# Kernel optimization log

Measured on AMD Instinct MI355X. Metric: run time of the kernel, lower is better.

Reference implementation:

```python
import jax, jax.numpy as jnp
import numpy as np

D_MODEL = 1024
N_HEAD = 16
HEAD_DIM = D_MODEL // N_HEAD


def setup_inputs() -> dict:
    key = jax.random.key(0)
    ks = jax.random.split(key, 11)
    B, S = 2, 2048
    scale = 1.0 / np.sqrt(D_MODEL)
    inp = {
        'q': jax.random.normal(ks[0], (B, S, D_MODEL), dtype=jnp.float32),
        'k': jax.random.normal(ks[1], (B, S, D_MODEL), dtype=jnp.float32),
        'v': jax.random.normal(ks[2], (B, S, D_MODEL), dtype=jnp.float32),
        'Wq': jax.random.normal(ks[3], (D_MODEL, D_MODEL), dtype=jnp.float32) * scale,
        'bq': jnp.zeros((D_MODEL,), dtype=jnp.float32),
        'Wk': jax.random.normal(ks[4], (D_MODEL, D_MODEL), dtype=jnp.float32) * scale,
        'bk': jnp.zeros((D_MODEL,), dtype=jnp.float32),
        'Wv': jax.random.normal(ks[5], (D_MODEL, D_MODEL), dtype=jnp.float32) * scale,
        'bv': jnp.zeros((D_MODEL,), dtype=jnp.float32),
        'Wo': jax.random.normal(ks[6], (D_MODEL, D_MODEL), dtype=jnp.float32) * scale,
        'bo': jnp.zeros((D_MODEL,), dtype=jnp.float32),
    }
    return inp


def _split_heads(x):
    # [B, S, D] -> [B, H, S, Dh]
    B, S, _ = x.shape
    return x.reshape(B, S, N_HEAD, HEAD_DIM).transpose(0, 2, 1, 3)


def reference(q, k, v, Wq, bq, Wk, bk, Wv, bv, Wo, bo):
    B, S, _ = q.shape
    qh = _split_heads(q @ Wq + bq)  # [B,H,S,Dh]
    kh = _split_heads(k @ Wk + bk)
    vh = _split_heads(v @ Wv + bv)
    inv_sqrt_d = jnp.asarray(1.0 / np.sqrt(HEAD_DIM), dtype=q.dtype)
    scores = jnp.einsum('bhqd,bhkd->bhqk', qh, kh) * inv_sqrt_d  # [B,H,S,S]
    attn = jax.nn.softmax(scores, axis=-1)
    out = jnp.einsum('bhqk,bhkd->bhqd', attn, vh)  # [B,H,S,Dh]
    out = out.transpose(0, 2, 1, 3).reshape(B, S, D_MODEL)
    return out @ Wo + bo
```

## Files before the change

### kernel.cpp

```cpp
#include <hip/hip_runtime.h>
#include <cstdint>
#include <cstddef>

#define D_MODEL 1024
#define NHEAD 16
#define HDIM 64
#define BATCH 2
#define SEQ 2048
#define MROWS (BATCH*SEQ)

typedef _Float16 f16;
typedef _Float16 f16x2 __attribute__((ext_vector_type(2)));
typedef _Float16 f16x4 __attribute__((ext_vector_type(4)));
typedef _Float16 f16x8 __attribute__((ext_vector_type(8)));
typedef float f32x4 __attribute__((ext_vector_type(4)));
typedef __fp16 fp16x2_raw __attribute__((ext_vector_type(2)));

__device__ __forceinline__ f16x2 cvt_pk(float a, float b) {
  fp16x2_raw t = __builtin_amdgcn_cvt_pkrtz(a, b);
  return __builtin_bit_cast(f16x2, t);
}

#define QSCALE 0.18033688011112042f
#define CSHIFT 6.0f

__device__ __forceinline__ void gload_lds16(const void* gsrc, void* ldst) {
  __builtin_amdgcn_global_load_lds(
      (__attribute__((address_space(1))) void*)gsrc,
      (__attribute__((address_space(3))) void*)ldst,
      16, 0, 0);
}

__global__ __launch_bounds__(256) void cast3_kernel(
    const float* __restrict__ q, const float* __restrict__ k,
    const float* __restrict__ v, f16* __restrict__ Xf) {
  const int z = blockIdx.y;
  const float* in = (z == 0) ? q : (z == 1) ? k : v;
  f16* out = Xf + (size_t)z * MROWS * D_MODEL;
  int i = (blockIdx.x * 256 + threadIdx.x) * 8;
  const float4* p = (const float4*)(in + i);
  float4 a = p[0], b = p[1];
  f16x8 o = { (f16)a.x,(f16)a.y,(f16)a.z,(f16)a.w,
              (f16)b.x,(f16)b.y,(f16)b.z,(f16)b.w };
  *(f16x8*)(out + i) = o;
}

__global__ __launch_bounds__(256) void transpose4_kernel(
    const float* __restrict__ W0, const float* __restrict__ W1,
    const float* __restrict__ W2, const float* __restrict__ W3,
    f16* __restrict__ T0, f16* __restrict__ T1,
    f16* __restrict__ T2, f16* __restrict__ T3) {
  const int z = blockIdx.z;
  const float* W = (z == 0) ? W0 : (z == 1) ? W1 : (z == 2) ? W2 : W3;
  f16* Wt = (z == 0) ? T0 : (z == 1) ? T1 : (z == 2) ? T2 : T3;
  __shared__ float tile[32][33];
  int n0 = blockIdx.x * 32, k0 = blockIdx.y * 32;
  int tx = threadIdx.x, ty = threadIdx.y;
  #pragma unroll
  for (int j = 0; j < 32; j += 8)
    tile[ty + j][tx] = W[(size_t)(k0 + ty + j) * D_MODEL + n0 + tx];
  __syncthreads();
  #pragma unroll
  for (int j = 0; j < 32; j += 8)
    Wt[(size_t)(n0 + ty + j) * D_MODEL + k0 + tx] = (f16)tile[tx][ty + j];
}

__global__ __launch_bounds__(256, 3) void gemm_qkv(
    const f16* __restrict__ Xf,
    const f16* __restrict__ Wtq, const f16* __restrict__ Wtk, const f16* __restrict__ Wtv,
    const float* __restrict__ bq, const float* __restrict__ bk, const float* __restrict__ bv,
    f16* __restrict__ Qh, f16* __restrict__ Kh, f16* __restrict__ Vt) {
  __shared__ __align__(16) f16 As[128 * 64];
  __shared__ __align__(16) f16 Bs[128 * 64];
  const int id = blockIdx.x;
  const int xcd = id & 7;
  const int s5 = id >> 3;
  const int bn_i = s5 & 7;
  const int t5 = xcd * 12 + (s5 >> 3);
  const int z = t5 >> 5;
  const int bm_i = t5 & 31;
  const int bm = bm_i * 128, bn = bn_i * 128;
  const f16* A  = Xf + (size_t)z * MROWS * D_MODEL + (size_t)bm * 1024;
  const f16* Bt = ((z == 0) ? Wtq : (z == 1) ? Wtk : Wtv) + (size_t)bn * 1024;
  const float* bias = (z == 0) ? bq : (z == 1) ? bk : bv;
  const int tid = threadIdx.x, wave = tid >> 6, lane = tid & 63;
  const int lr = lane & 15, lq = lane >> 4, sw = lr & 7;
  const int wm = (wave >> 1) * 64, wn = (wave & 1) * 64;
  const int srow = lane >> 3;
  const int scs  = (lane & 7) ^ srow;
  const f16* Ag = A  + (size_t)(wave * 32 + srow) * 1024 + scs * 8;
  const f16* Bg = Bt + (size_t)(wave * 32 + srow) * 1024 + scs * 8;

  f32x4 acc[4][4];
  #pragma unroll
  for (int i = 0; i < 4; i++)
    #pragma unroll
    for (int j = 0; j < 4; j++) acc[i][j] = (f32x4){0.f, 0.f, 0.f, 0.f};

  for (int k0 = 0; k0 < 1024; k0 += 64) {
    __syncthreads();
    #pragma unroll
    for (int g = 0; g < 4; g++) {
      gload_lds16(Ag + (size_t)g * 8 * 1024 + k0, As + wave * 2048 + g * 512);
      gload_lds16(Bg + (size_t)g * 8 * 1024 + k0, Bs + wave * 2048 + g * 512);
    }
    __syncthreads();
    #pragma unroll
    for (int t = 0; t < 2; t++) {
      f16x8 af[4], bf[4];
      #pragma unroll
      for (int m = 0; m < 4; m++)
        af[m] = *(const f16x8*)(As + (size_t)(wm + m * 16 + lr) * 64 + (((t * 4 + lq) ^ sw) * 8));
      #pragma unroll
      for (int j = 0; j < 4; j++)
        bf[j] = *(const f16x8*)(Bs + (size_t)(wn + j * 16 + lr) * 64 + (((t * 4 + lq) ^ sw) * 8));
      #pragma unroll
      for (int m = 0; m < 4; m++)
        #pragma unroll
        for (int j = 0; j < 4; j++)
          acc[m][j] = __builtin_amdgcn_mfma_f32_16x16x32_f16(af[m], bf[j], acc[m][j], 0, 0, 0);
    }
  }

  f16* dst = (z == 0) ? Qh : (z == 1) ? Kh : Vt;
  #pragma unroll
  for (int j = 0; j < 4; j++) {
    const int col = bn + wn + j * 16 + lr;
    const float bj = bias[col];
    const int hh = col >> 6, d = col & 63;
    #pragma unroll
    for (int m = 0; m < 4; m++) {
      #pragma unroll
      for (int r = 0; r < 4; r++) {
        const int row = bm + wm + m * 16 + lq * 4 + r;
        float val = acc[m][j][r] + bj;
        if (z == 0) val *= QSCALE;
        const int b = row >> 11, s = row & 2047;
        if (z != 2) {
          dst[(((size_t)b * NHEAD + hh) * SEQ + s) * HDIM + d] = (f16)val;
        } else {
          const int sp = (s & ~63) | (((s >> 4) & 1) << 5) | (((s >> 2) & 3) << 3)
                       | (((s >> 5) & 1) << 2) | (s & 3);
          dst[(((size_t)b * NHEAD + hh) * HDIM + d) * SEQ + sp] = (f16)val;
        }
      }
    }
  }
}

__global__ __launch_bounds__(256, 4) void gemm_o(
    const f16* __restrict__ AO, const f16* __restrict__ Wto,
    const float* __restrict__ bo, float* __restrict__ out) {
  __shared__ __align__(16) f16 As[64 * 64];
  __shared__ __align__(16) f16 Bs[128 * 64];
  const int id = blockIdx.x;
  const int xcd = id & 7;
  const int s5 = id >> 3;
  const int bn_i = s5 & 7;
  const int bm_i = xcd * 8 + (s5 >> 3);
  const int bm = bm_i * 64, bn = bn_i * 128;
  const int tid = threadIdx.x, wave = tid >> 6, lane = tid & 63;
  const int lr = lane & 15, lq = lane >> 4, sw = lr & 7;
  const int wm = (wave >> 1) * 32, wn = (wave & 1) * 64;
  const int srow = lane >> 3;
  const int scs  = (lane & 7) ^ srow;
  const f16* Ag = AO  + (size_t)(bm + wave * 16 + srow) * 1024 + scs * 8;
  const f16* Bg = Wto + (size_t)(bn + wave * 32 + srow) * 1024 + scs * 8;

  f32x4 acc[2][4];
  #pragma unroll
  for (int i = 0; i < 2; i++)
    #pragma unroll
    for (int j = 0; j < 4; j++) acc[i][j] = (f32x4){0.f, 0.f, 0.f, 0.f};

  for (int k0 = 0; k0 < 1024; k0 += 64) {
    __syncthreads();
    #pragma unroll
    for (int g = 0; g < 2; g++)
      gload_lds16(Ag + (size_t)g * 8 * 1024 + k0, As + wave * 1024 + g * 512);
    #pragma unroll
    for (int g = 0; g < 4; g++)
      gload_lds16(Bg + (size_t)g * 8 * 1024 + k0, Bs + wave * 2048 + g * 512);
    __syncthreads();
    #pragma unroll
    for (int t = 0; t < 2; t++) {
      f16x8 af[2], bf[4];
      #pragma unroll
      for (int m = 0; m < 2; m++)
        af[m] = *(const f16x8*)(As + (size_t)(wm + m * 16 + lr) * 64 + (((t * 4 + lq) ^ sw) * 8));
      #pragma unroll
      for (int j = 0; j < 4; j++)
        bf[j] = *(const f16x8*)(Bs + (size_t)(wn + j * 16 + lr) * 64 + (((t * 4 + lq) ^ sw) * 8));
      #pragma unroll
      for (int m = 0; m < 2; m++)
        #pragma unroll
        for (int j = 0; j < 4; j++)
          acc[m][j] = __builtin_amdgcn_mfma_f32_16x16x32_f16(af[m], bf[j], acc[m][j], 0, 0, 0);
    }
  }
  #pragma unroll
  for (int j = 0; j < 4; j++) {
    const int col = bn + wn + j * 16 + lr;
    const float bj = bo[col];
    #pragma unroll
    for (int m = 0; m < 2; m++)
      #pragma unroll
      for (int r = 0; r < 4; r++) {
        const int row = bm + wm + m * 16 + lq * 4 + r;
        out[(size_t)row * D_MODEL + col] = acc[m][j][r] + bj;
      }
  }
}

__global__ __launch_bounds__(256, 2) void flash_kernel(
    const f16* __restrict__ Qh, const f16* __restrict__ Kh,
    const f16* __restrict__ Vt, f16* __restrict__ AO) {
  __shared__ __align__(16) f16 Ks[2][64 * 64];
  __shared__ __align__(16) f16 Vs[2][64 * 64];
  const int id = blockIdx.x;
  const int xcd = id & 7;
  const int s5 = id >> 3;
  const int q_i = s5 & 15;
  const int hl = xcd * 4 + (s5 >> 4);
  const int h = hl & 15, b = hl >> 4;
  const int tid = threadIdx.x, wave = tid >> 6, lane = tid & 63;
  const int lr = lane & 15, lq = lane >> 4, sw = lr & 7;
  const f16* Qb = Qh + ((size_t)b * NHEAD + h) * SEQ * HDIM;
  const f16* Kb = Kh + ((size_t)b * NHEAD + h) * SEQ * HDIM;
  const f16* Vb = Vt + ((size_t)b * NHEAD + h) * HDIM * SEQ;
  const int q0 = q_i * 128 + wave * 32;

  f16x8 aq[2][2];
  #pragma unroll
  for (int m = 0; m < 2; m++)
    #pragma unroll
    for (int t = 0; t < 2; t++)
      aq[m][t] = *(const f16x8*)(Qb + (size_t)(q0 + m * 16 + lr) * HDIM + t * 32 + lq * 8);

  f32x4 oacc[2][4], ls[2];
  #pragma unroll
  for (int m = 0; m < 2; m++) {
    ls[m] = (f32x4){0.f, 0.f, 0.f, 0.f};
    #pragma unroll
    for (int j = 0; j < 4; j++) oacc[m][j] = (f32x4){0.f, 0.f, 0.f, 0.f};
  }
  const f32x4 mC = {-CSHIFT, -CSHIFT, -CSHIFT, -CSHIFT};
  const f16x8 ones = {(f16)1, (f16)1, (f16)1, (f16)1, (f16)1, (f16)1, (f16)1, (f16)1};

  const int krow = lane >> 3;
  const int kc   = (lane & 7) ^ krow;
  const f16* Kr0 = Kb + (size_t)(wave * 8 + krow) * HDIM + kc * 8;
  const f16* Kr1 = Kb + (size_t)(32 + wave * 8 + krow) * HDIM + kc * 8;
  const f16* Vr0 = Vb + (size_t)(wave * 8 + krow) * SEQ + kc * 8;
  const f16* Vr1 = Vb + (size_t)(32 + wave * 8 + krow) * SEQ + kc * 8;

  gload_lds16(Kr0, &Ks[0][wave * 512]);
  gload_lds16(Kr1, &Ks[0][2048 + wave * 512]);
  gload_lds16(Vr0, &Vs[0][wave * 512]);
  gload_lds16(Vr1, &Vs[0][2048 + wave * 512]);
  __syncthreads();

  for (int it2 = 0; it2 < 16; it2++) {
    #pragma unroll
    for (int hf = 0; hf < 2; hf++) {
      const int it = it2 * 2 + hf;
      const int kt = it * 64;

      if (it < 31) {
        gload_lds16(Kr0 + (size_t)(kt + 64) * HDIM, &Ks[hf ^ 1][wave * 512]);
        gload_lds16(Kr1 + (size_t)(kt + 64) * HDIM, &Ks[hf ^ 1][2048 + wave * 512]);
        gload_lds16(Vr0 + (kt + 64), &Vs[hf ^ 1][wave * 512]);
        gload_lds16(Vr1 + (kt + 64), &Vs[hf ^ 1][2048 + wave * 512]);
      }

      f16x8 bk[4][2];
      #pragma unroll
      for (int j = 0; j < 4; j++)
        #pragma unroll
        for (int t = 0; t < 2; t++)
          bk[j][t] = *(const f16x8*)(&Ks[hf][(size_t)(j * 16 + lr) * 64 + (((t * 4 + lq) ^ sw) * 8)]);
      f32x4 sc[4][2];
      #pragma unroll
      for (int j = 0; j < 4; j++)
        #pragma unroll
        for (int m = 0; m < 2; m++) {
          sc[j][m] = __builtin_amdgcn_mfma_f32_16x16x32_f16(bk[j][0], aq[m][0], mC, 0, 0, 0);
          sc[j][m] = __builtin_amdgcn_mfma_f32_16x16x32_f16(bk[j][1], aq[m][1], sc[j][m], 0, 0, 0);
        }

      f16x8 ap[2][2];
      #pragma unroll
      for (int m = 0; m < 2; m++)
        #pragma unroll
        for (int t = 0; t < 2; t++) {
          union { f16x8 v; f16x2 h2[4]; } u;
          const f32x4 lo = sc[t][m], hi = sc[t + 2][m];
          u.h2[0] = cvt_pk(exp2f(lo[0]), exp2f(lo[1]));
          u.h2[1] = cvt_pk(exp2f(lo[2]), exp2f(lo[3]));
          u.h2[2] = cvt_pk(exp2f(hi[0]), exp2f(hi[1]));
          u.h2[3] = cvt_pk(exp2f(hi[2]), exp2f(hi[3]));
          ap[m][t] = u.v;
        }

      #pragma unroll
      for (int t = 0; t < 2; t++) {
        #pragma unroll
        for (int j = 0; j < 4; j++) {
          f16x8 bv = *(const f16x8*)(&Vs[hf][(size_t)(j * 16 + lr) * 64 + (((t * 4 + lq) ^ sw) * 8)]);
          #pragma unroll
          for (int m = 0; m < 2; m++)
            oacc[m][j] = __builtin_amdgcn_mfma_f32_16x16x32_f16(ap[m][t], bv, oacc[m][j], 0, 0, 0);
        }
        #pragma unroll
        for (int m = 0; m < 2; m++)
          ls[m] = __builtin_amdgcn_mfma_f32_16x16x32_f16(ap[m][t], ones, ls[m], 0, 0, 0);
      }
      __syncthreads();
    }
  }

  #pragma unroll
  for (int m = 0; m < 2; m++)
    #pragma unroll
    for (int r = 0; r < 4; r++) {
      const float inv = 1.0f / ls[m][r];
      const int row = q0 + m * 16 + lq * 4 + r;
      #pragma unroll
      for (int j = 0; j < 4; j++) {
        const int col = h * HDIM + j * 16 + lr;
        AO[((size_t)b * SEQ + row) * D_MODEL + col] = (f16)(oacc[m][j][r] * inv);
      }
    }
}

extern "C" void kernel_launch(void* const* d_in, const int* in_sizes, int n_in,
                              void* d_out, int out_size, void* d_ws, size_t ws_size,
                              hipStream_t stream) {
  const float* q  = (const float*)d_in[0];
  const float* k  = (const float*)d_in[1];
  const float* v  = (const float*)d_in[2];
  const float* Wq = (const float*)d_in[3];
  const float* bq = (const float*)d_in[4];
  const float* Wk = (const float*)d_in[5];
  const float* bk = (const float*)d_in[6];
  const float* Wv = (const float*)d_in[7];
  const float* bv = (const float*)d_in[8];
  const float* Wo = (const float*)d_in[9];
  const float* bo = (const float*)d_in[10];
  float* out = (float*)d_out;

  char* ws = (char*)d_ws;
  f16* Wt_q = (f16*)(ws + ((size_t)0  << 20));
  f16* Wt_k = (f16*)(ws + ((size_t)2  << 20));
  f16* Wt_v = (f16*)(ws + ((size_t)4  << 20));
  f16* Wt_o = (f16*)(ws + ((size_t)6  << 20));
  f16* Xf   = (f16*)(ws + ((size_t)8  << 20));
  f16* Qh_  = (f16*)(ws + ((size_t)32 << 20));
  f16* Kh_  = (f16*)(ws + ((size_t)40 << 20));
  f16* Vt_  = (f16*)(ws + ((size_t)48 << 20));
  f16* AO   = Xf;

  transpose4_kernel<<<dim3(32, 32, 4), dim3(32, 8), 0, stream>>>(
      Wq, Wk, Wv, Wo, Wt_q, Wt_k, Wt_v, Wt_o);

  cast3_kernel<<<dim3(2048, 3), 256, 0, stream>>>(q, k, v, Xf);

  gemm_qkv<<<768, 256, 0, stream>>>(
      Xf, Wt_q, Wt_k, Wt_v, bq, bk, bv, Qh_, Kh_, Vt_);

  flash_kernel<<<512, 256, 0, stream>>>(Qh_, Kh_, Vt_, AO);

  gemm_o<<<512, 256, 0, stream>>>(AO, Wt_o, bo, out);
}
```

Baseline: 228.2 us.

## Halve flash attention block to two waves with 64 query rows and use native exp2

Flash attention blocks shrink from four waves (128 query rows) to two waves (64 rows), and the grid doubles to 1024 blocks. The block-to-head mapping is updated to match, and K/V staging is rewritten so that two waves load each 64-row tile with four loads per wave per tensor. exp2f is replaced by the hardware exp2 builtin to drop range handling. Smaller blocks raise the block count and possibly occupancy, but each K/V tile is now loaded into LDS for every 64 query rows, which doubles K/V global traffic and the loads per wave.

```diff
diff --git a/kernel.cpp b/kernel.cpp
--- a/kernel.cpp
+++ b/kernel.cpp
@@ -19,6 +19,10 @@
 __device__ __forceinline__ f16x2 cvt_pk(float a, float b) {
   fp16x2_raw t = __builtin_amdgcn_cvt_pkrtz(a, b);
   return __builtin_bit_cast(f16x2, t);
+}
+
+__device__ __forceinline__ float fast_exp2(float x) {
+  return __builtin_amdgcn_exp2f(x);
 }
 
 #define QSCALE 0.18033688011112042f
@@ -212,23 +216,23 @@
   }
 }
 
-__global__ __launch_bounds__(256, 2) void flash_kernel(
+__global__ __launch_bounds__(128, 4) void flash_kernel(
     const f16* __restrict__ Qh, const f16* __restrict__ Kh,
     const f16* __restrict__ Vt, f16* __restrict__ AO) {
   __shared__ __align__(16) f16 Ks[2][64 * 64];
   __shared__ __align__(16) f16 Vs[2][64 * 64];
   const int id = blockIdx.x;
   const int xcd = id & 7;
-  const int s5 = id >> 3;
-  const int q_i = s5 & 15;
-  const int hl = xcd * 4 + (s5 >> 4);
+  const int s7 = id >> 3;
+  const int q_i = s7 & 31;
+  const int hl = xcd * 4 + (s7 >> 5);
   const int h = hl & 15, b = hl >> 4;
   const int tid = threadIdx.x, wave = tid >> 6, lane = tid & 63;
   const int lr = lane & 15, lq = lane >> 4, sw = lr & 7;
   const f16* Qb = Qh + ((size_t)b * NHEAD + h) * SEQ * HDIM;
   const f16* Kb = Kh + ((size_t)b * NHEAD + h) * SEQ * HDIM;
   const f16* Vb = Vt + ((size_t)b * NHEAD + h) * HDIM * SEQ;
-  const int q0 = q_i * 128 + wave * 32;
+  const int q0 = q_i * 64 + wave * 32;
 
   f16x8 aq[2][2];
   #pragma unroll
@@ -249,29 +253,30 @@
 
   const int krow = lane >> 3;
   const int kc   = (lane & 7) ^ krow;
-  const f16* Kr0 = Kb + (size_t)(wave * 8 + krow) * HDIM + kc * 8;
-  const f16* Kr1 = Kb + (size_t)(32 + wave * 8 + krow) * HDIM + kc * 8;
-  const f16* Vr0 = Vb + (size_t)(wave * 8 + krow) * SEQ + kc * 8;
-  const f16* Vr1 = Vb + (size_t)(32 + wave * 8 + krow) * SEQ + kc * 8;
-
-  gload_lds16(Kr0, &Ks[0][wave * 512]);
-  gload_lds16(Kr1, &Ks[0][2048 + wave * 512]);
-  gload_lds16(Vr0, &Vs[0][wave * 512]);
-  gload_lds16(Vr1, &Vs[0][2048 + wave * 512]);
+  const f16* Kst = Kb + (size_t)(wave * 8 + krow) * HDIM + kc * 8;
+  const f16* Vst = Vb + (size_t)(wave * 8 + krow) * SEQ + kc * 8;
+
+  #define STAGE(it, bf)                                                        \
+    do {                                                                       \
+      _Pragma("unroll")                                                        \
+      for (int g = 0; g < 4; g++)                                              \
+        gload_lds16(Kst + (size_t)((it) * 64 + g * 16) * HDIM,                 \
+                    &Ks[bf][(g * 2 + wave) * 512]);                            \
+      _Pragma("unroll")                                                        \
+      for (int g = 0; g < 4; g++)                                              \
+        gload_lds16(Vst + (size_t)g * 16 * SEQ + (it) * 64,                    \
+                    &Vs[bf][(g * 2 + wave) * 512]);                            \
+    } while (0)
+
+  STAGE(0, 0);
   __syncthreads();
 
   for (int it2 = 0; it2 < 16; it2++) {
     #pragma unroll
     for (int hf = 0; hf < 2; hf++) {
       const int it = it2 * 2 + hf;
-      const int kt = it * 64;
-
-      if (it < 31) {
-        gload_lds16(Kr0 + (size_t)(kt + 64) * HDIM, &Ks[hf ^ 1][wave * 512]);
-        gload_lds16(Kr1 + (size_t)(kt + 64) * HDIM, &Ks[hf ^ 1][2048 + wave * 512]);
-        gload_lds16(Vr0 + (kt + 64), &Vs[hf ^ 1][wave * 512]);
-        gload_lds16(Vr1 + (kt + 64), &Vs[hf ^ 1][2048 + wave * 512]);
-      }
+
+      if (it < 31) STAGE(it + 1, hf ^ 1);
 
       f16x8 bk[4][2];
       #pragma unroll
@@ -295,10 +300,10 @@
         for (int t = 0; t < 2; t++) {
           union { f16x8 v; f16x2 h2[4]; } u;
           const f32x4 lo = sc[t][m], hi = sc[t + 2][m];
-          u.h2[0] = cvt_pk(exp2f(lo[0]), exp2f(lo[1]));
-          u.h2[1] = cvt_pk(exp2f(lo[2]), exp2f(lo[3]));
-          u.h2[2] = cvt_pk(exp2f(hi[0]), exp2f(hi[1]));
-          u.h2[3] = cvt_pk(exp2f(hi[2]), exp2f(hi[3]));
+          u.h2[0] = cvt_pk(fast_exp2(lo[0]), fast_exp2(lo[1]));
+          u.h2[1] = cvt_pk(fast_exp2(lo[2]), fast_exp2(lo[3]));
+          u.h2[2] = cvt_pk(fast_exp2(hi[0]), fast_exp2(hi[1]));
+          u.h2[3] = cvt_pk(fast_exp2(hi[2]), fast_exp2(hi[3]));
           ap[m][t] = u.v;
         }
 
@@ -318,6 +323,7 @@
       __syncthreads();
     }
   }
+  #undef STAGE
 
   #pragma unroll
   for (int m = 0; m < 2; m++)
@@ -368,7 +374,7 @@
   gemm_qkv<<<768, 256, 0, stream>>>(
       Xf, Wt_q, Wt_k, Wt_v, bq, bk, bv, Qh_, Kh_, Vt_);
 
-  flash_kernel<<<512, 256, 0, stream>>>(Qh_, Kh_, Vt_, AO);
+  flash_kernel<<<1024, 128, 0, stream>>>(Qh_, Kh_, Vt_, AO);
 
   gemm_o<<<512, 256, 0, stream>>>(AO, Wt_o, bo, out);
 }
```

Result: slower. 235.0 us (+3.0%).
